# Performance work log

Hardware: AMD Instinct MI355X
Metric: run time of the kernel (lower is better)

Reference implementation:

```python
import jax, jax.numpy as jnp
import numpy as np

B = 8192
INPUT_DIM = 1024
PATH_DIM = 256
HIDDEN_DIM = 1024
OUTPUT_DIM = 1024
STEPS = 50


def setup_inputs() -> dict:
    key = jax.random.key(0)
    ks = jax.random.split(key, 12)
    s = lambda fan_in: 1.0 / np.sqrt(fan_in)
    x0 = jax.random.normal(ks[0], (B, INPUT_DIM), dtype=jnp.float32)
    W_pe = jax.random.uniform(ks[1], (INPUT_DIM, PATH_DIM), jnp.float32, -s(INPUT_DIM), s(INPUT_DIM))
    b_pe = jax.random.uniform(ks[2], (PATH_DIM,), jnp.float32, -s(INPUT_DIM), s(INPUT_DIM))
    W_hi = jax.random.uniform(ks[3], (INPUT_DIM, HIDDEN_DIM), jnp.float32, -s(INPUT_DIM), s(INPUT_DIM))
    b_hi = jax.random.uniform(ks[4], (HIDDEN_DIM,), jnp.float32, -s(INPUT_DIM), s(INPUT_DIM))
    f_in = HIDDEN_DIM + PATH_DIM
    W1 = jax.random.uniform(ks[5], (f_in, HIDDEN_DIM), jnp.float32, -s(f_in), s(f_in))
    b1 = jax.random.uniform(ks[6], (HIDDEN_DIM,), jnp.float32, -s(f_in), s(f_in))
    W2 = jax.random.uniform(ks[7], (HIDDEN_DIM, HIDDEN_DIM), jnp.float32, -s(HIDDEN_DIM), s(HIDDEN_DIM))
    b2 = jax.random.uniform(ks[8], (HIDDEN_DIM,), jnp.float32, -s(HIDDEN_DIM), s(HIDDEN_DIM))
    W_ro = jax.random.uniform(ks[9], (HIDDEN_DIM, OUTPUT_DIM), jnp.float32, -s(HIDDEN_DIM), s(HIDDEN_DIM))
    b_ro = jax.random.uniform(ks[10], (OUTPUT_DIM,), jnp.float32, -s(HIDDEN_DIM), s(HIDDEN_DIM))
    return {"x0": x0, "W_pe": W_pe, "b_pe": b_pe, "W_hi": W_hi, "b_hi": b_hi,
            "W1": W1, "b1": b1, "W2": W2, "b2": b2, "W_ro": W_ro, "b_ro": b_ro}


def reference(x0, W_pe, b_pe, W_hi, b_hi, W1, b1, W2, b2, W_ro, b_ro):
    dt = 1.0 / float(STEPS)
    g = x0 @ W_pe + b_pe          # [B, path_dim]
    z0 = x0 @ W_hi + b_hi          # [B, hidden_dim]
    ts = dt * jnp.arange(1, STEPS + 1, dtype=jnp.float32)  # t after each step

    def step(z, t):
        u_t = t * g                                  # [B, path_dim]
        inp = jnp.concatenate([z, u_t], axis=-1)     # [B, hidden+path]
        dz = jnp.tanh(inp @ W1 + b1) @ W2 + b2       # [B, hidden_dim]
        return z + dt * dz, None

    z, _ = jax.lax.scan(step, z0, ts)
    return z @ W_ro + b_ro
```

## Files before the change

### kernel.cpp

```cpp
#include <hip/hip_runtime.h>
#include <hip/hip_bf16.h>

typedef __hip_bfloat16 bf16;
typedef __bf16 bf16x8 __attribute__((ext_vector_type(8)));
typedef float f32x4 __attribute__((ext_vector_type(4)));

#define ROWS   32
#define HID    1024
#define PATH   256
#define NSTEP  50
#define P      1032
#define SMEM_BYTES (2 * ROWS * P * 2)

__device__ __forceinline__ f32x4 mfma16(bf16x8 a, bf16x8 b, f32x4 c) {
    return __builtin_amdgcn_mfma_f32_16x16x32_bf16(a, b, c, 0, 0, 0);
}

__device__ __forceinline__ float tanh_fast(float x) {
    float e = __expf(2.0f * x);
    return 1.0f - 2.0f / (e + 1.0f);
}

__device__ __forceinline__ bf16x8 ldcvt8(const float* __restrict__ p) {
    f32x4 lo = *(const f32x4*)p;
    f32x4 hi = *(const f32x4*)(p + 4);
    bf16x8 r;
    #pragma unroll
    for (int j = 0; j < 4; j++) { r[j] = (__bf16)lo[j]; r[4 + j] = (__bf16)hi[j]; }
    return r;
}

__device__ __forceinline__ unsigned bfbits(float f) {
    __hip_bfloat16 h = __float2bfloat16(f);
    unsigned short u; __builtin_memcpy(&u, &h, 2);
    return (unsigned)u;
}
__device__ __forceinline__ unsigned bfpack2(float lo, float hi) {
    return bfbits(lo) | (bfbits(hi) << 16);
}
__device__ __forceinline__ float bflo(unsigned u) { return __uint_as_float(u << 16); }
__device__ __forceinline__ float bfhi(unsigned u) { return __uint_as_float(u & 0xffff0000u); }

__global__ void pack_frag(const float* __restrict__ src, bf16* __restrict__ dst, int N) {
    int kb = blockIdx.x, nb = blockIdx.y, l = threadIdx.x;
    int lm = l & 15, lq = l >> 4;
    bf16x8 v;
    #pragma unroll
    for (int j = 0; j < 8; j++)
        v[j] = __float2bfloat16(src[(size_t)(kb * 32 + lq * 8 + j) * N + nb * 16 + lm]);
    *(bf16x8*)(dst + ((size_t)(kb * gridDim.y + nb) * 64 + l) * 8) = v;
}

__device__ __forceinline__ void loadw4(const bf16* __restrict__ Wp, int k, int woff,
                                       bf16x8 (&w)[4]) {
    const bf16* wp = Wp + (size_t)k * 32768 + woff;
    #pragma unroll
    for (int nt = 0; nt < 4; nt++) w[nt] = *(const bf16x8*)(wp + nt * 512);
}

template<int KB>
__device__ __forceinline__ void gemm4d(const bf16* __restrict__ lds,
                                       const bf16* __restrict__ Wp,
                                       int wave, int lane, int krot,
                                       bf16x8 (&wA)[4], f32x4 (&acc)[2][4]) {
    static_assert((KB & (KB - 1)) == 0, "KB must be a power of two");
    const int lm = lane & 15, lq = lane >> 4;
    const bf16* a0b = lds + lm * P + lq * 8;
    const bf16* a1b = a0b + 16 * P;
    const int woff = wave * 2048 + lane * 8;

    bf16x8 wB[4];
    {
        const int k1 = (krot + 1) & (KB - 1);
        const bf16* wp = Wp + (size_t)k1 * 32768 + woff;
        #pragma unroll
        for (int nt = 0; nt < 4; nt++) wB[nt] = *(const bf16x8*)(wp + nt * 512);
    }
    const int k0 = krot & (KB - 1);
    bf16x8 a0 = *(const bf16x8*)(a0b + k0 * 32);
    bf16x8 a1 = *(const bf16x8*)(a1b + k0 * 32);

    #pragma unroll 1
    for (int kb = 0; kb < KB; kb += 2) {
        const int ka1 = (kb + 1 + krot) & (KB - 1);
        const int kw2 = (kb + 2 + krot) & (KB - 1);
        const int kw3 = (kb + 3 + krot) & (KB - 1);
        const bf16* wp2 = Wp + (size_t)kw2 * 32768 + woff;
        const bf16* wp3 = Wp + (size_t)kw3 * 32768 + woff;
        acc[0][0] = mfma16(a0, wA[0], acc[0][0]);
        acc[0][1] = mfma16(a0, wA[1], acc[0][1]);
        acc[0][2] = mfma16(a0, wA[2], acc[0][2]);
        acc[0][3] = mfma16(a0, wA[3], acc[0][3]);
        a0 = *(const bf16x8*)(a0b + ka1 * 32);
        acc[1][0] = mfma16(a1, wA[0], acc[1][0]);
        wA[0] = *(const bf16x8*)(wp2);
        acc[1][1] = mfma16(a1, wA[1], acc[1][1]);
        wA[1] = *(const bf16x8*)(wp2 + 512);
        acc[1][2] = mfma16(a1, wA[2], acc[1][2]);
        wA[2] = *(const bf16x8*)(wp2 + 1024);
        acc[1][3] = mfma16(a1, wA[3], acc[1][3]);
        wA[3] = *(const bf16x8*)(wp2 + 1536);
        a1 = *(const bf16x8*)(a1b + ka1 * 32);
        acc[0][0] = mfma16(a0, wB[0], acc[0][0]);
        acc[0][1] = mfma16(a0, wB[1], acc[0][1]);
        acc[0][2] = mfma16(a0, wB[2], acc[0][2]);
        acc[0][3] = mfma16(a0, wB[3], acc[0][3]);
        a0 = *(const bf16x8*)(a0b + kw2 * 32);
        acc[1][0] = mfma16(a1, wB[0], acc[1][0]);
        wB[0] = *(const bf16x8*)(wp3);
        acc[1][1] = mfma16(a1, wB[1], acc[1][1]);
        wB[1] = *(const bf16x8*)(wp3 + 512);
        acc[1][2] = mfma16(a1, wB[2], acc[1][2]);
        wB[2] = *(const bf16x8*)(wp3 + 1024);
        acc[1][3] = mfma16(a1, wB[3], acc[1][3]);
        wB[3] = *(const bf16x8*)(wp3 + 1536);
        a1 = *(const bf16x8*)(a1b + kw2 * 32);
    }
}

__global__ __launch_bounds__(1024, 4) void cde_main(
    const float* __restrict__ x0,  const float* __restrict__ b_pe, const float* __restrict__ b_hi,
    const float* __restrict__ b1v, const float* __restrict__ b2v,  const float* __restrict__ b_ro,
    const bf16* __restrict__ WpeP, const bf16* __restrict__ WhiP,
    const bf16* __restrict__ W1zP, const bf16* __restrict__ W1uP,
    const bf16* __restrict__ W2P,  const bf16* __restrict__ WroP,
    float* __restrict__ out)
{
    extern __shared__ bf16 smem[];
    bf16* inp = smem;
    bf16* th  = smem + ROWS * P;

    const int tid  = threadIdx.x;
    const int wave = tid >> 6;
    const int lane = tid & 63;
    const int lm   = lane & 15;
    const int lq   = lane >> 4;
    const int rot  = (blockIdx.x >> 3) & 31;
    const int krot = (rot + wave * 2) & 31;
    const int woff = wave * 2048 + lane * 8;
    const long row0 = (long)blockIdx.x * ROWS;

    f32x4 z[2][4];
    f32x4 g[2];
    uint2 cu_pk[2][4];

    #pragma unroll
    for (int nt = 0; nt < 4; nt++) {
        float b = b_hi[wave * 64 + nt * 16 + lm];
        #pragma unroll
        for (int r = 0; r < 4; r++) { z[0][nt][r] = b; z[1][nt][r] = b; }
    }
    {
        float b = b_pe[wave * 16 + lm];
        #pragma unroll
        for (int r = 0; r < 4; r++) { g[0][r] = b; g[1][r] = b; }
    }
    for (int kb = 0; kb < HID / 32; kb++) {
        int kbr = kb + krot; if (kbr >= 32) kbr -= 32;
        bf16x8 a0 = ldcvt8(x0 + (row0 +      lm) * HID + kbr * 32 + lq * 8);
        bf16x8 a1 = ldcvt8(x0 + (row0 + 16 + lm) * HID + kbr * 32 + lq * 8);
        const bf16* wp = WhiP + (((size_t)kbr * 64 + wave * 4) * 64 + lane) * 8;
        #pragma unroll
        for (int nt = 0; nt < 4; nt++) {
            bf16x8 bb = *(const bf16x8*)(wp + nt * 512);
            z[0][nt] = mfma16(a0, bb, z[0][nt]);
            z[1][nt] = mfma16(a1, bb, z[1][nt]);
        }
        bf16x8 pb = *(const bf16x8*)(WpeP + (((size_t)kbr * 16 + wave) * 64 + lane) * 8);
        g[0] = mfma16(a0, pb, g[0]);
        g[1] = mfma16(a1, pb, g[1]);
    }

    #pragma unroll
    for (int mt = 0; mt < 2; mt++)
        #pragma unroll
        for (int r = 0; r < 4; r++)
            inp[(mt * 16 + lq * 4 + r) * P + wave * 16 + lm] = __float2bfloat16(g[mt][r]);
    __syncthreads();
    {
        f32x4 cu[2][4];
        #pragma unroll
        for (int mt = 0; mt < 2; mt++)
            #pragma unroll
            for (int nt = 0; nt < 4; nt++)
                #pragma unroll
                for (int r = 0; r < 4; r++) cu[mt][nt][r] = 0.0f;
        for (int kb = 0; kb < PATH / 32; kb++) {
            const bf16* wp = W1uP + (((size_t)kb * 64 + wave * 4) * 64 + lane) * 8;
            bf16x8 a0 = *(const bf16x8*)(inp + lm * P + kb * 32 + lq * 8);
            bf16x8 a1 = *(const bf16x8*)(inp + (16 + lm) * P + kb * 32 + lq * 8);
            #pragma unroll
            for (int nt = 0; nt < 4; nt++) {
                bf16x8 bb = *(const bf16x8*)(wp + nt * 512);
                cu[0][nt] = mfma16(a0, bb, cu[0][nt]);
                cu[1][nt] = mfma16(a1, bb, cu[1][nt]);
            }
        }
        #pragma unroll
        for (int mt = 0; mt < 2; mt++)
            #pragma unroll
            for (int nt = 0; nt < 4; nt++)
                cu_pk[mt][nt] = make_uint2(bfpack2(cu[mt][nt][0], cu[mt][nt][1]),
                                           bfpack2(cu[mt][nt][2], cu[mt][nt][3]));
    }
    __syncthreads();

    const float DT = 1.0f / (float)NSTEP;

    unsigned b12[4];
    #pragma unroll
    for (int nt = 0; nt < 4; nt++)
        b12[nt] = bfpack2(b1v[wave * 64 + nt * 16 + lm],
                          DT * b2v[wave * 64 + nt * 16 + lm]);

    bf16x8 wpre[4];
    loadw4(W1zP, krot, woff, wpre);

    for (int s = 0; s < NSTEP; s++) {
        float t = DT * (float)(s + 1);

        #pragma unroll
        for (int mt = 0; mt < 2; mt++)
            #pragma unroll
            for (int nt = 0; nt < 4; nt++)
                #pragma unroll
                for (int r = 0; r < 4; r++)
                    inp[(mt * 16 + lq * 4 + r) * P + wave * 64 + nt * 16 + lm] =
                        __float2bfloat16(z[mt][nt][r]);
        __syncthreads();

        {
            f32x4 acc[2][4];
            #pragma unroll
            for (int mt = 0; mt < 2; mt++)
                #pragma unroll
                for (int nt = 0; nt < 4; nt++) {
                    float b1 = bflo(b12[nt]);
                    unsigned px = cu_pk[mt][nt].x, py = cu_pk[mt][nt].y;
                    acc[mt][nt][0] = fmaf(t, bflo(px), b1);
                    acc[mt][nt][1] = fmaf(t, bfhi(px), b1);
                    acc[mt][nt][2] = fmaf(t, bflo(py), b1);
                    acc[mt][nt][3] = fmaf(t, bfhi(py), b1);
                }
            gemm4d<HID / 32>(inp, W1zP, wave, lane, krot, wpre, acc);
            loadw4(W2P, krot, woff, wpre);
            #pragma unroll
            for (int mt = 0; mt < 2; mt++)
                #pragma unroll
                for (int nt = 0; nt < 4; nt++)
                    #pragma unroll
                    for (int r = 0; r < 4; r++)
                        th[(mt * 16 + lq * 4 + r) * P + wave * 64 + nt * 16 + lm] =
                            __float2bfloat16(DT * tanh_fast(acc[mt][nt][r]));
        }
        __syncthreads();

        {
            #pragma unroll
            for (int mt = 0; mt < 2; mt++)
                #pragma unroll
                for (int nt = 0; nt < 4; nt++) {
                    float db = bfhi(b12[nt]);
                    #pragma unroll
                    for (int r = 0; r < 4; r++) z[mt][nt][r] += db;
                }
            gemm4d<HID / 32>(th, W2P, wave, lane, krot, wpre, z);
            const bf16* nW = (s + 1 < NSTEP) ? W1zP : WroP;
            loadw4(nW, krot, woff, wpre);
        }
    }

    #pragma unroll
    for (int mt = 0; mt < 2; mt++)
        #pragma unroll
        for (int nt = 0; nt < 4; nt++)
            #pragma unroll
            for (int r = 0; r < 4; r++)
                inp[(mt * 16 + lq * 4 + r) * P + wave * 64 + nt * 16 + lm] =
                    __float2bfloat16(z[mt][nt][r]);
    __syncthreads();
    {
        f32x4 acc[2][4];
        #pragma unroll
        for (int nt = 0; nt < 4; nt++) {
            float b = b_ro[wave * 64 + nt * 16 + lm];
            #pragma unroll
            for (int r = 0; r < 4; r++) { acc[0][nt][r] = b; acc[1][nt][r] = b; }
        }
        gemm4d<HID / 32>(inp, WroP, wave, lane, krot, wpre, acc);
        #pragma unroll
        for (int mt = 0; mt < 2; mt++)
            #pragma unroll
            for (int nt = 0; nt < 4; nt++)
                #pragma unroll
                for (int r = 0; r < 4; r++)
                    out[(row0 + mt * 16 + lq * 4 + r) * HID + wave * 64 + nt * 16 + lm] =
                        acc[mt][nt][r];
    }
}

extern "C" void kernel_launch(void* const* d_in, const int* in_sizes, int n_in,
                              void* d_out, int out_size, void* d_ws, size_t ws_size,
                              hipStream_t stream) {
    (void)in_sizes; (void)n_in; (void)out_size; (void)ws_size;
    const float* x0  = (const float*)d_in[0];
    const float* Wpe = (const float*)d_in[1];
    const float* bpe = (const float*)d_in[2];
    const float* Whi = (const float*)d_in[3];
    const float* bhi = (const float*)d_in[4];
    const float* W1  = (const float*)d_in[5];
    const float* b1  = (const float*)d_in[6];
    const float* W2  = (const float*)d_in[7];
    const float* b2  = (const float*)d_in[8];
    const float* Wro = (const float*)d_in[9];
    const float* bro = (const float*)d_in[10];

    bf16* ws   = (bf16*)d_ws;
    bf16* WpeP = ws;
    bf16* WhiP = WpeP + 256 * 1024;
    bf16* W1zP = WhiP + 1024 * 1024;
    bf16* W1uP = W1zP + 1024 * 1024;
    bf16* W2P  = W1uP + 256 * 1024;
    bf16* WroP = W2P  + 1024 * 1024;

    hipLaunchKernelGGL(pack_frag, dim3(1024 / 32, 256 / 16), dim3(64), 0, stream, Wpe, WpeP, 256);
    hipLaunchKernelGGL(pack_frag, dim3(1024 / 32, 1024 / 16), dim3(64), 0, stream, Whi, WhiP, 1024);
    hipLaunchKernelGGL(pack_frag, dim3(1024 / 32, 1024 / 16), dim3(64), 0, stream, W1, W1zP, 1024);
    hipLaunchKernelGGL(pack_frag, dim3(256 / 32, 1024 / 16), dim3(64), 0, stream,
                       W1 + (size_t)1024 * 1024, W1uP, 1024);
    hipLaunchKernelGGL(pack_frag, dim3(1024 / 32, 1024 / 16), dim3(64), 0, stream, W2, W2P, 1024);
    hipLaunchKernelGGL(pack_frag, dim3(1024 / 32, 1024 / 16), dim3(64), 0, stream, Wro, WroP, 1024);

    hipFuncSetAttribute((const void*)cde_main,
                        hipFuncAttributeMaxDynamicSharedMemorySize, SMEM_BYTES);
    hipLaunchKernelGGL(cde_main, dim3(8192 / ROWS), dim3(1024), SMEM_BYTES, stream,
                       x0, bpe, bhi, b1, b2, bro, WpeP, WhiP, W1zP, W1uP, W2P, WroP,
                       (float*)d_out);
}
```

Before: 2.943 ms.

## Split each wave's 64-column GEMM into two 32-column passes with fewer live registers

Each per-step GEMM (W1z, W2, and the readout) now runs as two sequential passes over 32-column halves, using four accumulators per pass instead of eight. The aim is to lower VGPR pressure and shorten MFMA dependency chains, with two k-blocks of A and W prefetched and the loop tail peeled. The per-wave k-rotation is also dropped so all waves in a block start at the same k offset. In exchange, the A fragments are read from LDS twice per GEMM, and all waves hitting the same weight rows at once could increase L2 contention.

```diff
diff --git a/kernel.cpp b/kernel.cpp
--- a/kernel.cpp
+++ b/kernel.cpp
@@ -51,71 +51,75 @@
     *(bf16x8*)(dst + ((size_t)(kb * gridDim.y + nb) * 64 + l) * 8) = v;
 }
 
-__device__ __forceinline__ void loadw4(const bf16* __restrict__ Wp, int k, int woff,
-                                       bf16x8 (&w)[4]) {
-    const bf16* wp = Wp + (size_t)k * 32768 + woff;
-    #pragma unroll
-    for (int nt = 0; nt < 4; nt++) w[nt] = *(const bf16x8*)(wp + nt * 512);
+__device__ __forceinline__ void loadw_entry(const bf16* __restrict__ Wp, int krot,
+                                            int nboff, int lane, bf16x8 (&w)[4]) {
+    const bf16* b = Wp + nboff + lane * 8;
+    const int k1 = (krot + 1) & 31;
+    const bf16* p0 = b + (size_t)krot * 32768;
+    const bf16* p1 = b + (size_t)k1 * 32768;
+    w[0] = *(const bf16x8*)(p0);
+    w[1] = *(const bf16x8*)(p0 + 512);
+    w[2] = *(const bf16x8*)(p1);
+    w[3] = *(const bf16x8*)(p1 + 512);
+}
+
+__device__ __forceinline__ void init_acc(float t, float b1, uint2 cu, f32x4& c) {
+    c[0] = fmaf(t, bflo(cu.x), b1);
+    c[1] = fmaf(t, bfhi(cu.x), b1);
+    c[2] = fmaf(t, bflo(cu.y), b1);
+    c[3] = fmaf(t, bfhi(cu.y), b1);
 }
 
 template<int KB>
-__device__ __forceinline__ void gemm4d(const bf16* __restrict__ lds,
+__device__ __forceinline__ void gemm2p(const bf16* __restrict__ lds,
                                        const bf16* __restrict__ Wp,
-                                       int wave, int lane, int krot,
-                                       bf16x8 (&wA)[4], f32x4 (&acc)[2][4]) {
+                                       int lane, int krot, int nboff,
+                                       bf16x8 (&wE)[4],
+                                       f32x4& c00, f32x4& c01, f32x4& c10, f32x4& c11) {
     static_assert((KB & (KB - 1)) == 0, "KB must be a power of two");
     const int lm = lane & 15, lq = lane >> 4;
     const bf16* a0b = lds + lm * P + lq * 8;
     const bf16* a1b = a0b + 16 * P;
-    const int woff = wave * 2048 + lane * 8;
-
-    bf16x8 wB[4];
-    {
-        const int k1 = (krot + 1) & (KB - 1);
-        const bf16* wp = Wp + (size_t)k1 * 32768 + woff;
-        #pragma unroll
-        for (int nt = 0; nt < 4; nt++) wB[nt] = *(const bf16x8*)(wp + nt * 512);
-    }
+    const bf16* wb = Wp + nboff + lane * 8;
+
     const int k0 = krot & (KB - 1);
-    bf16x8 a0 = *(const bf16x8*)(a0b + k0 * 32);
-    bf16x8 a1 = *(const bf16x8*)(a1b + k0 * 32);
+    const int k1 = (krot + 1) & (KB - 1);
+    bf16x8 a0A = *(const bf16x8*)(a0b + k0 * 32);
+    bf16x8 a1A = *(const bf16x8*)(a1b + k0 * 32);
+    bf16x8 a0B = *(const bf16x8*)(a0b + k1 * 32);
+    bf16x8 a1B = *(const bf16x8*)(a1b + k1 * 32);
 
     #pragma unroll 1
-    for (int kb = 0; kb < KB; kb += 2) {
-        const int ka1 = (kb + 1 + krot) & (KB - 1);
+    for (int kb = 0; kb < KB - 2; kb += 2) {
         const int kw2 = (kb + 2 + krot) & (KB - 1);
         const int kw3 = (kb + 3 + krot) & (KB - 1);
-        const bf16* wp2 = Wp + (size_t)kw2 * 32768 + woff;
-        const bf16* wp3 = Wp + (size_t)kw3 * 32768 + woff;
-        acc[0][0] = mfma16(a0, wA[0], acc[0][0]);
-        acc[0][1] = mfma16(a0, wA[1], acc[0][1]);
-        acc[0][2] = mfma16(a0, wA[2], acc[0][2]);
-        acc[0][3] = mfma16(a0, wA[3], acc[0][3]);
-        a0 = *(const bf16x8*)(a0b + ka1 * 32);
-        acc[1][0] = mfma16(a1, wA[0], acc[1][0]);
-        wA[0] = *(const bf16x8*)(wp2);
-        acc[1][1] = mfma16(a1, wA[1], acc[1][1]);
-        wA[1] = *(const bf16x8*)(wp2 + 512);
-        acc[1][2] = mfma16(a1, wA[2], acc[1][2]);
-        wA[2] = *(const bf16x8*)(wp2 + 1024);
-        acc[1][3] = mfma16(a1, wA[3], acc[1][3]);
-        wA[3] = *(const bf16x8*)(wp2 + 1536);
-        a1 = *(const bf16x8*)(a1b + ka1 * 32);
-        acc[0][0] = mfma16(a0, wB[0], acc[0][0]);
-        acc[0][1] = mfma16(a0, wB[1], acc[0][1]);
-        acc[0][2] = mfma16(a0, wB[2], acc[0][2]);
-        acc[0][3] = mfma16(a0, wB[3], acc[0][3]);
-        a0 = *(const bf16x8*)(a0b + kw2 * 32);
-        acc[1][0] = mfma16(a1, wB[0], acc[1][0]);
-        wB[0] = *(const bf16x8*)(wp3);
-        acc[1][1] = mfma16(a1, wB[1], acc[1][1]);
-        wB[1] = *(const bf16x8*)(wp3 + 512);
-        acc[1][2] = mfma16(a1, wB[2], acc[1][2]);
-        wB[2] = *(const bf16x8*)(wp3 + 1024);
-        acc[1][3] = mfma16(a1, wB[3], acc[1][3]);
-        wB[3] = *(const bf16x8*)(wp3 + 1536);
-        a1 = *(const bf16x8*)(a1b + kw2 * 32);
-    }
+        const bf16* wp2 = wb + (size_t)kw2 * 32768;
+        const bf16* wp3 = wb + (size_t)kw3 * 32768;
+        c00 = mfma16(a0A, wE[0], c00);
+        c10 = mfma16(a1A, wE[0], c10);
+        wE[0] = *(const bf16x8*)(wp2);
+        c01 = mfma16(a0A, wE[1], c01);
+        c11 = mfma16(a1A, wE[1], c11);
+        wE[1] = *(const bf16x8*)(wp2 + 512);
+        a0A = *(const bf16x8*)(a0b + kw2 * 32);
+        a1A = *(const bf16x8*)(a1b + kw2 * 32);
+        c00 = mfma16(a0B, wE[2], c00);
+        c10 = mfma16(a1B, wE[2], c10);
+        wE[2] = *(const bf16x8*)(wp3);
+        c01 = mfma16(a0B, wE[3], c01);
+        c11 = mfma16(a1B, wE[3], c11);
+        wE[3] = *(const bf16x8*)(wp3 + 512);
+        a0B = *(const bf16x8*)(a0b + kw3 * 32);
+        a1B = *(const bf16x8*)(a1b + kw3 * 32);
+    }
+    c00 = mfma16(a0A, wE[0], c00);
+    c10 = mfma16(a1A, wE[0], c10);
+    c01 = mfma16(a0A, wE[1], c01);
+    c11 = mfma16(a1A, wE[1], c11);
+    c00 = mfma16(a0B, wE[2], c00);
+    c10 = mfma16(a1B, wE[2], c10);
+    c01 = mfma16(a0B, wE[3], c01);
+    c11 = mfma16(a1B, wE[3], c11);
 }
 
 __global__ __launch_bounds__(1024, 4) void cde_main(
@@ -136,8 +140,8 @@
     const int lm   = lane & 15;
     const int lq   = lane >> 4;
     const int rot  = (blockIdx.x >> 3) & 31;
-    const int krot = (rot + wave * 2) & 31;
-    const int woff = wave * 2048 + lane * 8;
+    const int nb0  = wave * 2048;
+    const int nb1  = wave * 2048 + 1024;
     const long row0 = (long)blockIdx.x * ROWS;
 
     f32x4 z[2][4];
@@ -156,7 +160,7 @@
         for (int r = 0; r < 4; r++) { g[0][r] = b; g[1][r] = b; }
     }
     for (int kb = 0; kb < HID / 32; kb++) {
-        int kbr = kb + krot; if (kbr >= 32) kbr -= 32;
+        int kbr = kb + rot; if (kbr >= 32) kbr -= 32;
         bf16x8 a0 = ldcvt8(x0 + (row0 +      lm) * HID + kbr * 32 + lq * 8);
         bf16x8 a1 = ldcvt8(x0 + (row0 + 16 + lm) * HID + kbr * 32 + lq * 8);
         const bf16* wp = WhiP + (((size_t)kbr * 64 + wave * 4) * 64 + lane) * 8;
@@ -213,8 +217,8 @@
         b12[nt] = bfpack2(b1v[wave * 64 + nt * 16 + lm],
                           DT * b2v[wave * 64 + nt * 16 + lm]);
 
-    bf16x8 wpre[4];
-    loadw4(W1zP, krot, woff, wpre);
+    bf16x8 wE[4], wE2[4];
+    loadw_entry(W1zP, rot, nb0, lane, wE);
 
     for (int s = 0; s < NSTEP; s++) {
         float t = DT * (float)(s + 1);
@@ -229,44 +233,64 @@
                         __float2bfloat16(z[mt][nt][r]);
         __syncthreads();
 
+        loadw_entry(W1zP, rot, nb1, lane, wE2);
+
         {
-            f32x4 acc[2][4];
-            #pragma unroll
-            for (int mt = 0; mt < 2; mt++)
-                #pragma unroll
-                for (int nt = 0; nt < 4; nt++) {
-                    float b1 = bflo(b12[nt]);
-                    unsigned px = cu_pk[mt][nt].x, py = cu_pk[mt][nt].y;
-                    acc[mt][nt][0] = fmaf(t, bflo(px), b1);
-                    acc[mt][nt][1] = fmaf(t, bfhi(px), b1);
-                    acc[mt][nt][2] = fmaf(t, bflo(py), b1);
-                    acc[mt][nt][3] = fmaf(t, bfhi(py), b1);
-                }
-            gemm4d<HID / 32>(inp, W1zP, wave, lane, krot, wpre, acc);
-            loadw4(W2P, krot, woff, wpre);
-            #pragma unroll
-            for (int mt = 0; mt < 2; mt++)
-                #pragma unroll
-                for (int nt = 0; nt < 4; nt++)
-                    #pragma unroll
-                    for (int r = 0; r < 4; r++)
-                        th[(mt * 16 + lq * 4 + r) * P + wave * 64 + nt * 16 + lm] =
-                            __float2bfloat16(DT * tanh_fast(acc[mt][nt][r]));
+            f32x4 c00, c01, c10, c11;
+            init_acc(t, bflo(b12[0]), cu_pk[0][0], c00);
+            init_acc(t, bflo(b12[1]), cu_pk[0][1], c01);
+            init_acc(t, bflo(b12[0]), cu_pk[1][0], c10);
+            init_acc(t, bflo(b12[1]), cu_pk[1][1], c11);
+            gemm2p<HID / 32>(inp, W1zP, lane, rot, nb0, wE, c00, c01, c10, c11);
+            bf16* tb = th + wave * 64 + lm;
+            #pragma unroll
+            for (int r = 0; r < 4; r++) {
+                tb[(lq * 4 + r) * P]           = __float2bfloat16(DT * tanh_fast(c00[r]));
+                tb[(lq * 4 + r) * P + 16]      = __float2bfloat16(DT * tanh_fast(c01[r]));
+                tb[(16 + lq * 4 + r) * P]      = __float2bfloat16(DT * tanh_fast(c10[r]));
+                tb[(16 + lq * 4 + r) * P + 16] = __float2bfloat16(DT * tanh_fast(c11[r]));
+            }
+        }
+        {
+            f32x4 c00, c01, c10, c11;
+            init_acc(t, bflo(b12[2]), cu_pk[0][2], c00);
+            init_acc(t, bflo(b12[3]), cu_pk[0][3], c01);
+            init_acc(t, bflo(b12[2]), cu_pk[1][2], c10);
+            init_acc(t, bflo(b12[3]), cu_pk[1][3], c11);
+            gemm2p<HID / 32>(inp, W1zP, lane, rot, nb1, wE2, c00, c01, c10, c11);
+            loadw_entry(W2P, rot, nb0, lane, wE);
+            bf16* tb = th + wave * 64 + 32 + lm;
+            #pragma unroll
+            for (int r = 0; r < 4; r++) {
+                tb[(lq * 4 + r) * P]           = __float2bfloat16(DT * tanh_fast(c00[r]));
+                tb[(lq * 4 + r) * P + 16]      = __float2bfloat16(DT * tanh_fast(c01[r]));
+                tb[(16 + lq * 4 + r) * P]      = __float2bfloat16(DT * tanh_fast(c10[r]));
+                tb[(16 + lq * 4 + r) * P + 16] = __float2bfloat16(DT * tanh_fast(c11[r]));
+            }
         }
         __syncthreads();
 
+        loadw_entry(W2P, rot, nb1, lane, wE2);
+
         {
-            #pragma unroll
-            for (int mt = 0; mt < 2; mt++)
-                #pragma unroll
-                for (int nt = 0; nt < 4; nt++) {
-                    float db = bfhi(b12[nt]);
-                    #pragma unroll
-                    for (int r = 0; r < 4; r++) z[mt][nt][r] += db;
-                }
-            gemm4d<HID / 32>(th, W2P, wave, lane, krot, wpre, z);
+            float d0 = bfhi(b12[0]), d1 = bfhi(b12[1]);
+            #pragma unroll
+            for (int r = 0; r < 4; r++) {
+                z[0][0][r] += d0; z[0][1][r] += d1;
+                z[1][0][r] += d0; z[1][1][r] += d1;
+            }
+            gemm2p<HID / 32>(th, W2P, lane, rot, nb0, wE, z[0][0], z[0][1], z[1][0], z[1][1]);
+        }
+        {
+            float d2 = bfhi(b12[2]), d3 = bfhi(b12[3]);
+            #pragma unroll
+            for (int r = 0; r < 4; r++) {
+                z[0][2][r] += d2; z[0][3][r] += d3;
+                z[1][2][r] += d2; z[1][3][r] += d3;
+            }
+            gemm2p<HID / 32>(th, W2P, lane, rot, nb1, wE2, z[0][2], z[0][3], z[1][2], z[1][3]);
             const bf16* nW = (s + 1 < NSTEP) ? W1zP : WroP;
-            loadw4(nW, krot, woff, wpre);
+            loadw_entry(nW, rot, nb0, lane, wE);
         }
     }
 
@@ -279,23 +303,34 @@
                 inp[(mt * 16 + lq * 4 + r) * P + wave * 64 + nt * 16 + lm] =
                     __float2bfloat16(z[mt][nt][r]);
     __syncthreads();
+    loadw_entry(WroP, rot, nb1, lane, wE2);
     {
-        f32x4 acc[2][4];
-        #pragma unroll
-        for (int nt = 0; nt < 4; nt++) {
-            float b = b_ro[wave * 64 + nt * 16 + lm];
-            #pragma unroll
-            for (int r = 0; r < 4; r++) { acc[0][nt][r] = b; acc[1][nt][r] = b; }
-        }
-        gemm4d<HID / 32>(inp, WroP, wave, lane, krot, wpre, acc);
-        #pragma unroll
-        for (int mt = 0; mt < 2; mt++)
-            #pragma unroll
-            for (int nt = 0; nt < 4; nt++)
-                #pragma unroll
-                for (int r = 0; r < 4; r++)
-                    out[(row0 + mt * 16 + lq * 4 + r) * HID + wave * 64 + nt * 16 + lm] =
-                        acc[mt][nt][r];
+        f32x4 c00, c01, c10, c11;
+        float br0 = b_ro[wave * 64 + lm], br1 = b_ro[wave * 64 + 16 + lm];
+        #pragma unroll
+        for (int r = 0; r < 4; r++) { c00[r] = br0; c01[r] = br1; c10[r] = br0; c11[r] = br1; }
+        gemm2p<HID / 32>(inp, WroP, lane, rot, nb0, wE, c00, c01, c10, c11);
+        #pragma unroll
+        for (int r = 0; r < 4; r++) {
+            out[(row0 + lq * 4 + r) * HID + wave * 64 + lm]           = c00[r];
+            out[(row0 + lq * 4 + r) * HID + wave * 64 + 16 + lm]      = c01[r];
+            out[(row0 + 16 + lq * 4 + r) * HID + wave * 64 + lm]      = c10[r];
+            out[(row0 + 16 + lq * 4 + r) * HID + wave * 64 + 16 + lm] = c11[r];
+        }
+    }
+    {
+        f32x4 c00, c01, c10, c11;
+        float br2 = b_ro[wave * 64 + 32 + lm], br3 = b_ro[wave * 64 + 48 + lm];
+        #pragma unroll
+        for (int r = 0; r < 4; r++) { c00[r] = br2; c01[r] = br3; c10[r] = br2; c11[r] = br3; }
+        gemm2p<HID / 32>(inp, WroP, lane, rot, nb1, wE2, c00, c01, c10, c11);
+        #pragma unroll
+        for (int r = 0; r < 4; r++) {
+            out[(row0 + lq * 4 + r) * HID + wave * 64 + 32 + lm]      = c00[r];
+            out[(row0 + lq * 4 + r) * HID + wave * 64 + 48 + lm]      = c01[r];
+            out[(row0 + 16 + lq * 4 + r) * HID + wave * 64 + 32 + lm] = c10[r];
+            out[(row0 + 16 + lq * 4 + r) * HID + wave * 64 + 48 + lm] = c11[r];
+        }
     }
 }
 
```

Measured after the change: 2.570 ms (median of 2 runs). -12.7%, faster.
